# Kernel optimization log

Hardware: AMD Instinct MI355X
Metric: run time of the kernel (lower is better)

The kernel has to match this reference:

```python
import jax, jax.numpy as jnp
import numpy as np
from jax import lax

N_ENT = 20000; N_REL = 256; H = 512; C = 64; K = 3; L = 2; T = 8; E = 30000; B = 4096


def _seg_mean(vals, ids, num_segments):
    s = jax.ops.segment_sum(vals, ids, num_segments=num_segments)
    c = jax.ops.segment_sum(jnp.ones(ids.shape, vals.dtype), ids, num_segments=num_segments)
    return s / jnp.maximum(c, 1.0)[:, None]


def _normalize(x, eps=1e-8):
    return x / (jnp.linalg.norm(x, axis=-1, keepdims=True) + eps)


def _gru(x, h, Wih, Whh, bih, bhh):
    gi = x @ Wih + bih
    gh = h @ Whh + bhh
    ir, iz, inn = jnp.split(gi, 3, axis=-1)
    hr, hz, hn = jnp.split(gh, 3, axis=-1)
    r = jax.nn.sigmoid(ir + hr)
    z = jax.nn.sigmoid(iz + hz)
    n = jnp.tanh(inn + r * hn)
    return (1.0 - z) * n + z * h


def _backbone(x, convW, convB, fcW, fcB):
    # x: (B, Cin, H) -> (B, H); ConvTrans backbone: 1D 'same' conv over hidden dim,
    # relu, flatten, linear projection back to H, relu (BN identity at init, dropout=eval)
    h = lax.conv_general_dilated(x, convW, (1,), 'SAME', dimension_numbers=('NCH', 'OIH', 'NCH'))
    h = jax.nn.relu(h + convB[None, :, None])
    h = h.reshape(h.shape[0], -1)
    return jax.nn.relu(h @ fcW + fcB)


def _forward(ent_embeds, rel_embeds, W_msg, W_self, gru_Wih, gru_Whh, gru_bih, gru_bhh,
             gate_W, gate_b,
             e_conv1, e_cb1, e_fc1, e_fb1, e_conv2, e_cb2, e_fc2, e_fb2,
             r_conv1, r_cb1, r_fc1, r_fb1, r_conv2, r_cb2, r_fc2, r_fb2,
             src, dst, erel, subj, rel, obj):
    def step(carry, xs):
        ent, relh = carry
        s, d, r = xs
        # relation evolution: aggregate incident-entity embeds per relation, GRU with static rel embeds
        agg = _seg_mean(ent[s], r, N_REL)                                   # (R, H)
        relh = _gru(jnp.concatenate([agg, rel_embeds], -1), relh, gru_Wih, gru_Whh, gru_bih, gru_bhh)
        # entity evolution: L layers of RGCN-style message passing over the snapshot
        h = ent
        for l in range(L):
            msg = (h[s] + relh[r]) @ W_msg[l]                               # (E, H)
            h = jax.nn.relu(_seg_mean(msg, d, N_ENT) + h @ W_self[l])
        h = _normalize(h)
        u = jax.nn.sigmoid(h @ gate_W + gate_b)                             # time gate
        ent = u * h + (1.0 - u) * ent
        return (ent, relh), None

    (ent, relh), _ = lax.scan(step, (_normalize(ent_embeds), rel_embeds), (src, dst, erel))

    se = ent[subj]
    re_ = relh[rel]
    oe = ent[obj]
    # RefineConvTransE (object prediction)
    o1 = _backbone(jnp.stack([se, re_], 1), e_conv1, e_cb1, e_fc1, e_fb1)
    o2 = _backbone(jnp.stack([o1, se, re_], 1), e_conv2, e_cb2, e_fc2, e_fb2)
    # RefineConvTransR (relation prediction)
    q1 = _backbone(jnp.stack([se, oe], 1), r_conv1, r_cb1, r_fc1, r_fb1)
    q2 = _backbone(jnp.stack([q1, se, oe], 1), r_conv2, r_cb2, r_fc2, r_fb2)
    return (o1 @ ent.T, q1 @ relh.T, o2 @ ent.T, q2 @ relh.T)


def setup_inputs() -> dict:
    key = jax.random.key(0)
    ks = jax.random.split(key, 32)
    f = lambda i, shape, s=0.02: jax.random.normal(ks[i], shape, jnp.float32) * s
    return dict(
        ent_embeds=f(0, (N_ENT, H), 0.05),
        rel_embeds=f(1, (N_REL, H), 0.05),
        W_msg=f(2, (L, H, H)),
        W_self=f(3, (L, H, H)),
        gru_Wih=f(4, (2 * H, 3 * H)),
        gru_Whh=f(5, (H, 3 * H)),
        gru_bih=jnp.zeros((3 * H,), jnp.float32),
        gru_bhh=jnp.zeros((3 * H,), jnp.float32),
        gate_W=f(6, (H, H)),
        gate_b=jnp.zeros((H,), jnp.float32),
        e_conv1=f(7, (C, 2, K)), e_cb1=jnp.zeros((C,), jnp.float32),
        e_fc1=f(8, (C * H, H)), e_fb1=jnp.zeros((H,), jnp.float32),
        e_conv2=f(9, (C, 3, K)), e_cb2=jnp.zeros((C,), jnp.float32),
        e_fc2=f(10, (C * H, H)), e_fb2=jnp.zeros((H,), jnp.float32),
        r_conv1=f(11, (C, 2, K)), r_cb1=jnp.zeros((C,), jnp.float32),
        r_fc1=f(12, (C * H, H)), r_fb1=jnp.zeros((H,), jnp.float32),
        r_conv2=f(13, (C, 3, K)), r_cb2=jnp.zeros((C,), jnp.float32),
        r_fc2=f(14, (C * H, H)), r_fb2=jnp.zeros((H,), jnp.float32),
        src=jax.random.randint(ks[15], (T, E), 0, N_ENT),
        dst=jax.random.randint(ks[16], (T, E), 0, N_ENT),
        erel=jax.random.randint(ks[17], (T, E), 0, N_REL),
        subj=jax.random.randint(ks[18], (B,), 0, N_ENT),
        rel=jax.random.randint(ks[19], (B,), 0, N_REL),
        obj=jax.random.randint(ks[20], (B,), 0, N_ENT),
    )


def reference(ent_embeds, rel_embeds, W_msg, W_self, gru_Wih, gru_Whh, gru_bih, gru_bhh,
              gate_W, gate_b,
              e_conv1, e_cb1, e_fc1, e_fb1, e_conv2, e_cb2, e_fc2, e_fb2,
              r_conv1, r_cb1, r_fc1, r_fb1, r_conv2, r_cb2, r_fc2, r_fb2,
              src, dst, erel, subj, rel, obj):
    # returns (obj_logit_ori, rel_logit_ori, obj_logit, rel_logit)
    return _forward(ent_embeds, rel_embeds, W_msg, W_self, gru_Wih, gru_Whh, gru_bih, gru_bhh,
                    gate_W, gate_b,
                    e_conv1, e_cb1, e_fc1, e_fb1, e_conv2, e_cb2, e_fc2, e_fb2,
                    r_conv1, r_cb1, r_fc1, r_fb1, r_conv2, r_cb2, r_fc2, r_fb2,
                    src, dst, erel, subj, rel, obj)
```

## Files before the change

kernel.cpp:

```cpp
#include <hip/hip_runtime.h>
#include <math.h>


#define N_ENT 20000
#define N_REL 256
#define HD    512
#define NE    30000
#define NB    4096
#define NT    8

typedef __attribute__((ext_vector_type(8))) short          bf16x8;
typedef __attribute__((ext_vector_type(4))) float          f32x4;
typedef __attribute__((ext_vector_type(8))) unsigned short u16x8;
typedef __attribute__((ext_vector_type(4))) unsigned short u16x4;

static __device__ __forceinline__ float sigmoidf_(float x) {
  return 1.0f / (1.0f + expf(-x));
}
static __device__ __forceinline__ unsigned short f2bf(float f) {
  unsigned u = __float_as_uint(f);
  return (unsigned short)((u + 0x7FFFu + ((u >> 16) & 1u)) >> 16);
}

__global__ void rownorm_kernel(const float* __restrict__ in, float* __restrict__ out,
                               unsigned short* __restrict__ outb, int rows) {
  int wid = (blockIdx.x * blockDim.x + threadIdx.x) >> 6;
  int lane = threadIdx.x & 63;
  if (wid >= rows) return;
  const float4* ip = (const float4*)(in + (size_t)wid * HD);
  float4 v0 = ip[lane];
  float4 v1 = ip[lane + 64];
  float s = v0.x * v0.x + v0.y * v0.y + v0.z * v0.z + v0.w * v0.w
          + v1.x * v1.x + v1.y * v1.y + v1.z * v1.z + v1.w * v1.w;
  #pragma unroll
  for (int m = 1; m < 64; m <<= 1) s += __shfl_xor(s, m);
  float inv = 1.0f / (sqrtf(s) + 1e-8f);
  float4* op = (float4*)(out + (size_t)wid * HD);
  v0.x *= inv; v0.y *= inv; v0.z *= inv; v0.w *= inv;
  v1.x *= inv; v1.y *= inv; v1.z *= inv; v1.w *= inv;
  op[lane] = v0; op[lane + 64] = v1;
  unsigned short* ob = outb + (size_t)wid * HD;
  u16x4 p0 = {f2bf(v0.x), f2bf(v0.y), f2bf(v0.z), f2bf(v0.w)};
  u16x4 p1 = {f2bf(v1.x), f2bf(v1.y), f2bf(v1.z), f2bf(v1.w)};
  *(u16x4*)&ob[lane * 4] = p0;
  *(u16x4*)&ob[(lane + 64) * 4] = p1;
}

__global__ void zero_hist_all(int* __restrict__ h) {
  int i = blockIdx.x * 256 + threadIdx.x;
  if (i < NT * (N_ENT + N_REL)) h[i] = 0;
}

__global__ void hist_all(const int* __restrict__ dst, const int* __restrict__ rel,
                         int* __restrict__ histD8, int* __restrict__ histR8) {
  int e = blockIdx.x * 256 + threadIdx.x;
  int t = blockIdx.y;
  if (e >= NE) return;
  atomicAdd(&histD8[t * N_ENT + dst[t * NE + e]], 1);
  atomicAdd(&histR8[t * N_REL + rel[t * NE + e]], 1);
}

__global__ void scan_part_all(const int* __restrict__ histD8, int* __restrict__ partD8) {
  int t = blockIdx.x, tid = threadIdx.x;
  const int* hd = histD8 + t * N_ENT;
  int base = tid * 80;
  int s = 0;
  for (int i = 0; i < 80; ++i) {
    int idx = base + i;
    if (idx < N_ENT) s += hd[idx];
  }
  partD8[t * 257 + tid] = s;
}

__global__ void scan_serial_all(int* __restrict__ partD8, const int* __restrict__ histR8,
                                int* __restrict__ startR8, int* __restrict__ posR8) {
  int t = blockIdx.x;
  int* pd = partD8 + t * 257;
  int run = 0;
  for (int i = 0; i < 256; ++i) { int v = pd[i]; pd[i] = run; run += v; }
  pd[256] = run;
  const int* hr = histR8 + t * N_REL;
  int* sr = startR8 + t * 257;
  int* pr = posR8 + t * N_REL;
  run = 0;
  for (int i = 0; i < 256; ++i) { int v = hr[i]; sr[i] = run; pr[i] = run; run += v; }
  sr[256] = run;
}

__global__ void scan_local_all(const int* __restrict__ histD8, const int* __restrict__ partD8,
                               int* __restrict__ startD8, int* __restrict__ posD8) {
  int t = blockIdx.x, tid = threadIdx.x;
  const int* hd = histD8 + t * N_ENT;
  int* sd = startD8 + t * (N_ENT + 1);
  int* pd = posD8 + t * N_ENT;
  int run = partD8[t * 257 + tid];
  int base = tid * 80;
  for (int i = 0; i < 80; ++i) {
    int idx = base + i;
    if (idx < N_ENT) {
      sd[idx] = run;
      pd[idx] = run;
      run += hd[idx];
    }
  }
  if (tid == 0) sd[N_ENT] = partD8[t * 257 + 256];
}

__global__ void scatter_all(const int* __restrict__ dst, const int* __restrict__ rel,
                            int* __restrict__ posD8, int* __restrict__ posR8,
                            int* __restrict__ edgeD8, int* __restrict__ edgeR8) {
  int e = blockIdx.x * 256 + threadIdx.x;
  int t = blockIdx.y;
  if (e >= NE) return;
  int p = atomicAdd(&posD8[t * N_ENT + dst[t * NE + e]], 1);
  edgeD8[t * NE + p] = e;
  int p2 = atomicAdd(&posR8[t * N_REL + rel[t * NE + e]], 1);
  edgeR8[t * NE + p2] = e;
}

__global__ __launch_bounds__(256)
void agg_rel_csr(const float* __restrict__ ent, const int* __restrict__ src,
                 const int* __restrict__ edgeR, const int* __restrict__ startR,
                 float* __restrict__ aggR, float* __restrict__ cntR) {
  int r = blockIdx.x * 4 + (threadIdx.x >> 6);
  if (r >= N_REL) return;
  int lane = threadIdx.x & 63;
  int s0 = startR[r], s1 = startR[r + 1];
  float4 a = make_float4(0.f, 0.f, 0.f, 0.f);
  float4 b = make_float4(0.f, 0.f, 0.f, 0.f);
  for (int i = s0; i < s1; ++i) {
    int e = edgeR[i];
    int s = src[e];
    const float4* p = (const float4*)(ent + (size_t)s * HD);
    float4 x = p[lane];
    float4 y = p[lane + 64];
    a.x += x.x; a.y += x.y; a.z += x.z; a.w += x.w;
    b.x += y.x; b.y += y.y; b.z += y.z; b.w += y.w;
  }
  float4* op = (float4*)(aggR + (size_t)r * HD);
  op[lane] = a;
  op[lane + 64] = b;
  if (lane == 0) cntR[r] = (float)(s1 - s0);
}

__global__ __launch_bounds__(256)
void agg_ent_csr(const float* __restrict__ h, const float* __restrict__ relh,
                 const int* __restrict__ src, const int* __restrict__ erel,
                 const int* __restrict__ edgeD, const int* __restrict__ startD,
                 float* __restrict__ aggE, float* __restrict__ cntE) {
  int d = blockIdx.x * 4 + (threadIdx.x >> 6);
  if (d >= N_ENT) return;
  int lane = threadIdx.x & 63;
  int s0 = startD[d], s1 = startD[d + 1];
  float4 a = make_float4(0.f, 0.f, 0.f, 0.f);
  float4 b = make_float4(0.f, 0.f, 0.f, 0.f);
  for (int i = s0; i < s1; ++i) {
    int e = edgeD[i];
    int s = src[e], r = erel[e];
    const float4* hp = (const float4*)(h + (size_t)s * HD);
    const float4* rp = (const float4*)(relh + (size_t)r * HD);
    float4 x = hp[lane];
    float4 y = hp[lane + 64];
    float4 u = rp[lane];
    float4 v = rp[lane + 64];
    a.x += x.x + u.x; a.y += x.y + u.y; a.z += x.z + u.z; a.w += x.w + u.w;
    b.x += y.x + v.x; b.y += y.y + v.y; b.z += y.z + v.z; b.w += y.w + v.w;
  }
  float4* op = (float4*)(aggE + (size_t)d * HD);
  op[lane] = a;
  op[lane + 64] = b;
  if (lane == 0) cntE[d] = (float)(s1 - s0);
}

__global__ void gru_kernel(const float* __restrict__ gi, const float* __restrict__ gh,
                           const float* __restrict__ bih, const float* __restrict__ bhh,
                           float* __restrict__ relh, unsigned short* __restrict__ relhb) {
  int i = blockIdx.x * blockDim.x + threadIdx.x;
  if (i >= N_REL * HD) return;
  int row = i >> 9, col = i & 511;
  const float* gir = gi + (size_t)row * 1536;
  const float* ghr = gh + (size_t)row * 1536;
  float ir = gir[col] + bih[col];
  float iz = gir[col + 512] + bih[col + 512];
  float inn = gir[col + 1024] + bih[col + 1024];
  float hr = ghr[col] + bhh[col];
  float hz = ghr[col + 512] + bhh[col + 512];
  float hn = ghr[col + 1024] + bhh[col + 1024];
  float r = sigmoidf_(ir + hr);
  float z = sigmoidf_(iz + hz);
  float n = tanhf(inn + r * hn);
  float v = (1.0f - z) * n + z * relh[i];
  relh[i] = v;
  relhb[i] = f2bf(v);
}

__global__ void gather_kernel(const float* __restrict__ table, const int* __restrict__ idx,
                              float* __restrict__ out, int rows) {
  int i = blockIdx.x * blockDim.x + threadIdx.x;
  if (i >= rows * (HD / 4)) return;
  int row = i >> 7, q = i & 127;
  ((float4*)out)[i] = ((const float4*)(table + (size_t)idx[row] * HD))[q];
}

__global__ void f2b_kernel(const float* __restrict__ in, unsigned short* __restrict__ out, int n) {
  int i = blockIdx.x * blockDim.x + threadIdx.x;
  if (i * 8 >= n) return;
  float4 a = *(const float4*)&in[i * 8];
  float4 b = *(const float4*)&in[i * 8 + 4];
  u16x8 pk = {f2bf(a.x), f2bf(a.y), f2bf(a.z), f2bf(a.w),
              f2bf(b.x), f2bf(b.y), f2bf(b.z), f2bf(b.w)};
  *(u16x8*)&out[i * 8] = pk;
}

__global__ void pack_nn_kernel(const float* __restrict__ B, unsigned short* __restrict__ out,
                               int K, int N) {
  int id = blockIdx.x * 256 + threadIdx.x;
  if (id >= (K >> 3) * N) return;
  int s = id / (N * 4);
  int rem = id - s * (N * 4);
  int n = rem >> 2, g = rem & 3;
  const float* src = B + (size_t)(s * 32 + g * 8) * N + n;
  u16x8 pk;
  #pragma unroll
  for (int j = 0; j < 8; ++j) pk[j] = f2bf(src[(size_t)j * N]);
  *(u16x8*)&out[((size_t)s * N + n) * 32 + ((g ^ ((n >> 2) & 3)) << 3)] = pk;
}

template <int ACT, int MIRROR>
static __device__ __forceinline__
void gemm_core(const float* __restrict__ A0, int K0, const float* __restrict__ cntA,
               const unsigned short* __restrict__ A1, int K1,
               const unsigned short* __restrict__ Bp,
               const float* __restrict__ bias, const float* __restrict__ D,
               float* __restrict__ C, unsigned short* __restrict__ Cb,
               int M, int N, int m0, int n0,
               unsigned short (*As)[8192], unsigned short (*Bs)[8192]) {
  const int tid = threadIdx.x;
  const int lane = tid & 63;
  const int wv = tid >> 6;
  const int wm = wv >> 1, wn = wv & 1;
  const int lr = lane & 15, lg = lane >> 4;
  const int arow = tid >> 1;
  const int akh = (tid & 1) * 32;
  const int achunk = (tid & 1) * 4;
  const int NIT = (K0 + K1) >> 6;

  float s0 = 1.0f;
  if (K0 > 0 && (m0 + arow) < M) s0 = 1.0f / fmaxf(cntA[m0 + arow], 1.0f);

  f32x4 acc[4][4];
  #pragma unroll
  for (int i = 0; i < 4; ++i)
    #pragma unroll
    for (int j = 0; j < 4; ++j) acc[i][j] = (f32x4){0.f, 0.f, 0.f, 0.f};

  auto gload = [&](int it, u16x8* ar, u16x8* br) {
    int mrow = m0 + arow;
    int kk = it * 64 + akh;
    if (mrow < M) {
      if (kk < K0) {
        const float* p = A0 + (size_t)mrow * K0 + kk;
        #pragma unroll
        for (int q = 0; q < 4; ++q) {
          float4 x = *(const float4*)(p + q * 8);
          float4 y = *(const float4*)(p + q * 8 + 4);
          ar[q] = (u16x8){f2bf(x.x * s0), f2bf(x.y * s0), f2bf(x.z * s0), f2bf(x.w * s0),
                          f2bf(y.x * s0), f2bf(y.y * s0), f2bf(y.z * s0), f2bf(y.w * s0)};
        }
      } else {
        const unsigned short* p = A1 + (size_t)mrow * K1 + (kk - K0);
        #pragma unroll
        for (int q = 0; q < 4; ++q) ar[q] = *(const u16x8*)&p[q * 8];
      }
    } else {
      #pragma unroll
      for (int q = 0; q < 4; ++q) ar[q] = (u16x8){0, 0, 0, 0, 0, 0, 0, 0};
    }
    const unsigned short* b0 = Bp + ((size_t)(2 * it) * N + n0) * 32;
    const unsigned short* b1 = Bp + ((size_t)(2 * it + 1) * N + n0) * 32;
    br[0] = *(const u16x8*)&b0[tid * 8];
    br[1] = *(const u16x8*)&b0[2048 + tid * 8];
    br[2] = *(const u16x8*)&b1[tid * 8];
    br[3] = *(const u16x8*)&b1[2048 + tid * 8];
  };
  auto swrite = [&](int nb, const u16x8* ar, const u16x8* br) {
    #pragma unroll
    for (int q = 0; q < 4; ++q) {
      int chunk = achunk + q;
      *(u16x8*)&As[nb][arow * 64 + ((chunk ^ (arow & 7)) << 3)] = ar[q];
    }
    *(u16x8*)&Bs[nb][tid * 8] = br[0];
    *(u16x8*)&Bs[nb][2048 + tid * 8] = br[1];
    *(u16x8*)&Bs[nb][4096 + tid * 8] = br[2];
    *(u16x8*)&Bs[nb][4096 + 2048 + tid * 8] = br[3];
  };

  {
    u16x8 ar[4], br[4];
    gload(0, ar, br);
    swrite(0, ar, br);
  }
  __syncthreads();

  int cur = 0;
  for (int it = 0; it < NIT; ++it) {
    u16x8 ar[4], br[4];
    if (it + 1 < NIT) gload(it + 1, ar, br);
    bf16x8 af[2][4], bfr[2][4];
    #pragma unroll
    for (int u = 0; u < 2; ++u)
      #pragma unroll
      for (int i = 0; i < 4; ++i) {
        int r = wm * 64 + i * 16 + lr;
        af[u][i] = *(const bf16x8*)&As[cur][r * 64 + (((u * 4 + lg) ^ (r & 7)) << 3)];
        int nl = wn * 64 + i * 16 + lr;
        bfr[u][i] = *(const bf16x8*)&Bs[cur][u * 4096 + nl * 32 + ((lg ^ ((nl >> 2) & 3)) << 3)];
      }
    #pragma unroll
    for (int u = 0; u < 2; ++u)
      #pragma unroll
      for (int i = 0; i < 4; ++i)
        #pragma unroll
        for (int j = 0; j < 4; ++j)
          acc[i][j] = __builtin_amdgcn_mfma_f32_16x16x32_bf16(af[u][i], bfr[u][j], acc[i][j], 0, 0, 0);
    if (it + 1 < NIT) swrite(cur ^ 1, ar, br);
    __syncthreads();
    cur ^= 1;
  }

  #pragma unroll
  for (int i = 0; i < 4; ++i) {
    int m = m0 + wm * 64 + i * 16 + lg * 4;
    #pragma unroll
    for (int j = 0; j < 4; ++j) {
      int n = n0 + wn * 64 + j * 16 + lr;
      #pragma unroll
      for (int q = 0; q < 4; ++q) {
        int mr = m + q;
        if (mr >= M) continue;
        size_t o = (size_t)mr * N + n;
        float v = acc[i][j][q];
        if (ACT == 0) {
          C[o] = v;
        } else if (ACT == 1) {
          float rr = fmaxf(v, 0.0f);
          C[o] = rr;
          if (MIRROR) Cb[o] = f2bf(rr);
        } else {
          float u_ = sigmoidf_(v + bias[n]);
          float rr = u_ * D[o] + (1.0f - u_) * C[o];
          C[o] = rr;
          if (MIRROR) Cb[o] = f2bf(rr);
        }
      }
    }
  }
}

template <int ACT, int MIRROR>
__global__ __launch_bounds__(256, 2)
void gemm_nn2(const float* __restrict__ A0, int K0, const float* __restrict__ cntA,
              const unsigned short* __restrict__ A1, int K1,
              const unsigned short* __restrict__ Bp,
              const float* __restrict__ bias, const float* __restrict__ D,
              float* __restrict__ C, unsigned short* __restrict__ Cb, int M, int N) {
  __shared__ unsigned short As[2][8192];
  __shared__ unsigned short Bs[2][8192];
  gemm_core<ACT, MIRROR>(A0, K0, cntA, A1, K1, Bp, bias, D, C, Cb, M, N,
                         blockIdx.x * 128, blockIdx.y * 128, As, Bs);
}

__global__ __launch_bounds__(256, 2)
void gru_gemms(const float* __restrict__ aggR, const float* __restrict__ cntR,
               const unsigned short* __restrict__ rel_bf,
               const unsigned short* __restrict__ relh_bf,
               const unsigned short* __restrict__ wp_ih,
               const unsigned short* __restrict__ wp_hh,
               float* __restrict__ gi, float* __restrict__ gh) {
  __shared__ unsigned short As[2][8192];
  __shared__ unsigned short Bs[2][8192];
  if (blockIdx.z == 0)
    gemm_core<0, 0>(aggR, 512, cntR, rel_bf, 512, wp_ih, nullptr, nullptr,
                    gi, nullptr, N_REL, 1536, blockIdx.x * 128, blockIdx.y * 128, As, Bs);
  else
    gemm_core<0, 0>(nullptr, 0, nullptr, relh_bf, 512, wp_hh, nullptr, nullptr,
                    gh, nullptr, N_REL, 1536, blockIdx.x * 128, blockIdx.y * 128, As, Bs);
}

__global__ __launch_bounds__(256)
void pack_fw_kernel(const float* __restrict__ f0, const float* __restrict__ f1,
                    const float* __restrict__ f2, const float* __restrict__ f3,
                    unsigned short* __restrict__ o0, unsigned short* __restrict__ o1,
                    unsigned short* __restrict__ o2, unsigned short* __restrict__ o3) {
  __shared__ float L[32][512];
  const float* fw; unsigned short* op;
  switch (blockIdx.y) {
    case 0: fw = f0; op = o0; break;
    case 1: fw = f1; op = o1; break;
    case 2: fw = f2; op = o2; break;
    default: fw = f3; op = o3; break;
  }
  int s = blockIdx.x, tid = threadIdx.x;
  #pragma unroll
  for (int i = 0; i < 16; ++i) {
    int idx = tid + 256 * i;
    int r = idx >> 7, cq = (idx & 127) << 2;
    *(float4*)&L[r][cq] = *(const float4*)&fw[(size_t)(s * 32 + r) * 512 + cq];
  }
  __syncthreads();
  #pragma unroll
  for (int ii = 0; ii < 8; ++ii) {
    int slot = tid + 256 * ii;
    int n = slot >> 2, g = slot & 3;
    u16x8 pk;
    #pragma unroll
    for (int j = 0; j < 8; ++j) pk[j] = f2bf(L[g * 8 + j][n]);
    size_t off = (size_t)s * 16384 + n * 32 + ((g ^ ((n >> 2) & 3)) << 3);
    *(u16x8*)&op[off] = pk;
  }
}

template <int CIN>
__global__ __launch_bounds__(256)
void convgen_kernel(const float* __restrict__ X0e, const float* __restrict__ X1e,
                    const float* __restrict__ X2e,
                    const float* __restrict__ cwE, const float* __restrict__ cbE,
                    const float* __restrict__ X0r, const float* __restrict__ X1r,
                    const float* __restrict__ X2r,
                    const float* __restrict__ cwR, const float* __restrict__ cbR,
                    unsigned short* __restrict__ Ae, unsigned short* __restrict__ Ar) {
  __shared__ float wsm[64 * CIN * 3];
  __shared__ float bsm[64];
  const int path = blockIdx.y;
  const float* X[CIN]; const float* cw; const float* cb; unsigned short* A;
  if (path == 0) {
    X[0] = X0e; X[1] = X1e; if constexpr (CIN == 3) X[2] = X2e;
    cw = cwE; cb = cbE; A = Ae;
  } else {
    X[0] = X0r; X[1] = X1r; if constexpr (CIN == 3) X[2] = X2r;
    cw = cwR; cb = cbR; A = Ar;
  }
  const int tid = threadIdx.x;
  for (int i = tid; i < 64 * CIN * 3; i += 256) wsm[i] = cw[i];
  if (tid < 64) bsm[tid] = cb[tid];
  __syncthreads();

  const int o = tid & 63;
  const int b = blockIdx.x * 4 + (tid >> 6);
  const int h = o * 8;

  float xm[CIN][8], xl[CIN], xr[CIN];
  #pragma unroll
  for (int ci = 0; ci < CIN; ++ci) {
    const float* row = X[ci] + (size_t)b * HD + h;
    float4 a4 = *(const float4*)row;
    float4 b4 = *(const float4*)(row + 4);
    xm[ci][0] = a4.x; xm[ci][1] = a4.y; xm[ci][2] = a4.z; xm[ci][3] = a4.w;
    xm[ci][4] = b4.x; xm[ci][5] = b4.y; xm[ci][6] = b4.z; xm[ci][7] = b4.w;
    xl[ci] = (h > 0) ? row[-1] : 0.f;
    xr[ci] = (h + 8 < HD) ? row[8] : 0.f;
  }
  unsigned short* dst = A + (size_t)b * 32768 + h;
  for (int c = 0; c < 64; ++c) {
    float v[8];
    float cbv = bsm[c];
    #pragma unroll
    for (int e = 0; e < 8; ++e) v[e] = cbv;
    #pragma unroll
    for (int ci = 0; ci < CIN; ++ci) {
      float w0 = wsm[(c * CIN + ci) * 3 + 0];
      float w1 = wsm[(c * CIN + ci) * 3 + 1];
      float w2 = wsm[(c * CIN + ci) * 3 + 2];
      #pragma unroll
      for (int e = 0; e < 8; ++e) {
        float lft = e ? xm[ci][e - 1] : xl[ci];
        float rgt = (e < 7) ? xm[ci][e + 1] : xr[ci];
        v[e] = fmaf(lft, w0, fmaf(xm[ci][e], w1, fmaf(rgt, w2, v[e])));
      }
    }
    u16x8 pk;
    #pragma unroll
    for (int e = 0; e < 8; ++e) pk[e] = f2bf(fmaxf(v[e], 0.f));
    *(u16x8*)&dst[c * 512] = pk;
  }
}

__global__ __launch_bounds__(256, 2)
void gemm_fc(const unsigned short* __restrict__ Abuf,
             const unsigned short* __restrict__ fwpE,
             const unsigned short* __restrict__ fwpR,
             float* __restrict__ partBase) {
  __shared__ unsigned short As[2][128 * 64];
  __shared__ unsigned short Bs[2][2 * 128 * 32];
  const int tid = threadIdx.x;
  const int lane = tid & 63;
  const int wv = tid >> 6;
  const int wm = wv >> 1, wn = wv & 1;
  const int lr = lane & 15, lg = lane >> 4;
  const int m0 = blockIdx.x * 128;
  const int n0 = blockIdx.y * 128;
  const int path = blockIdx.z >> 2;
  const int ks = blockIdx.z & 3;

  const unsigned short* A = Abuf + (size_t)path * ((size_t)NB * 32768);
  const unsigned short* fwp = (path == 0) ? fwpE : fwpR;
  float* part = partBase + (size_t)(path * 4 + ks) * ((size_t)NB * HD);

  const int arow = tid >> 1;
  const int achunk = (tid & 1) * 4;
  const unsigned short* aRow = A + (size_t)(m0 + arow) * 32768 + ks * 8192 + achunk * 8;
  const unsigned short* bBase = fwp + (size_t)(ks * 256) * 16384 + (size_t)n0 * 32;

  f32x4 acc[4][4];
  #pragma unroll
  for (int i = 0; i < 4; ++i)
    #pragma unroll
    for (int j = 0; j < 4; ++j) acc[i][j] = (f32x4){0.f, 0.f, 0.f, 0.f};

  auto gload = [&](int it, u16x8* ar, u16x8* br) {
    const unsigned short* ap = aRow + it * 64;
    #pragma unroll
    for (int q = 0; q < 4; ++q) ar[q] = *(const u16x8*)&ap[q * 8];
    const unsigned short* bp = bBase + (size_t)it * 2 * 16384;
    br[0] = *(const u16x8*)&bp[tid * 8];
    br[1] = *(const u16x8*)&bp[2048 + tid * 8];
    br[2] = *(const u16x8*)&bp[16384 + tid * 8];
    br[3] = *(const u16x8*)&bp[16384 + 2048 + tid * 8];
  };
  auto swrite = [&](int nb, const u16x8* ar, const u16x8* br) {
    #pragma unroll
    for (int q = 0; q < 4; ++q) {
      int chunk = achunk + q;
      *(u16x8*)&As[nb][arow * 64 + ((chunk ^ (arow & 7)) << 3)] = ar[q];
    }
    *(u16x8*)&Bs[nb][tid * 8] = br[0];
    *(u16x8*)&Bs[nb][2048 + tid * 8] = br[1];
    *(u16x8*)&Bs[nb][4096 + tid * 8] = br[2];
    *(u16x8*)&Bs[nb][4096 + 2048 + tid * 8] = br[3];
  };
  auto mfma_phase = [&](int nb) {
    bf16x8 af[2][4], bfr[2][4];
    #pragma unroll
    for (int u = 0; u < 2; ++u)
      #pragma unroll
      for (int i = 0; i < 4; ++i) {
        int r = wm * 64 + i * 16 + lr;
        af[u][i] = *(const bf16x8*)&As[nb][r * 64 + (((u * 4 + lg) ^ (r & 7)) << 3)];
        int nl = wn * 64 + i * 16 + lr;
        bfr[u][i] = *(const bf16x8*)&Bs[nb][u * 4096 + nl * 32 + ((lg ^ ((nl >> 2) & 3)) << 3)];
      }
    #pragma unroll
    for (int u = 0; u < 2; ++u)
      #pragma unroll
      for (int i = 0; i < 4; ++i)
        #pragma unroll
        for (int j = 0; j < 4; ++j)
          acc[i][j] = __builtin_amdgcn_mfma_f32_16x16x32_bf16(af[u][i], bfr[u][j], acc[i][j], 0, 0, 0);
  };

  u16x8 ar0[4], br0[4], ar1[4], br1[4];
  gload(0, ar0, br0);
  swrite(0, ar0, br0);
  gload(1, ar1, br1);
  __syncthreads();

  int cur = 0;
  for (int itp = 0; itp < 128; itp += 2) {
    if (itp + 2 < 128) gload(itp + 2, ar0, br0);
    mfma_phase(cur);
    swrite(cur ^ 1, ar1, br1);
    __syncthreads();
    cur ^= 1;
    if (itp + 3 < 128) gload(itp + 3, ar1, br1);
    mfma_phase(cur);
    if (itp + 2 < 128) swrite(cur ^ 1, ar0, br0);
    __syncthreads();
    cur ^= 1;
  }

  #pragma unroll
  for (int i = 0; i < 4; ++i) {
    int m = m0 + wm * 64 + i * 16 + lg * 4;
    #pragma unroll
    for (int j = 0; j < 4; ++j) {
      int n = n0 + wn * 64 + j * 16 + lr;
      #pragma unroll
      for (int q = 0; q < 4; ++q)
        part[(size_t)(m + q) * HD + n] = acc[i][j][q];
    }
  }
}

__global__ void reduce4_kernel(const float* __restrict__ pE, const float* __restrict__ pR,
                               const float* __restrict__ bE, const float* __restrict__ bR,
                               float* __restrict__ oE, float* __restrict__ oR,
                               unsigned short* __restrict__ obE, unsigned short* __restrict__ obR) {
  int p = blockIdx.y;
  const float* part = p ? pR : pE;
  const float* bias = p ? bR : bE;
  float* o = p ? oR : oE;
  unsigned short* ob = p ? obR : obE;
  int i = blockIdx.x * 256 + threadIdx.x;
  int col = (i << 2) & 511;
  float4 s = *(const float4*)&part[(size_t)i * 4];
  #pragma unroll
  for (int ks = 1; ks < 4; ++ks) {
    float4 t = *(const float4*)&part[(size_t)ks * (NB * HD) + i * 4];
    s.x += t.x; s.y += t.y; s.z += t.z; s.w += t.w;
  }
  float4 b4 = *(const float4*)&bias[col];
  s.x = fmaxf(s.x + b4.x, 0.f); s.y = fmaxf(s.y + b4.y, 0.f);
  s.z = fmaxf(s.z + b4.z, 0.f); s.w = fmaxf(s.w + b4.w, 0.f);
  *(float4*)&o[(size_t)i * 4] = s;
  u16x4 pk = {f2bf(s.x), f2bf(s.y), f2bf(s.z), f2bf(s.w)};
  *(u16x4*)&ob[(size_t)i * 4] = pk;
}

__global__ __launch_bounds__(256, 3)
void gemm_nt_bf16(const unsigned short* __restrict__ A, const unsigned short* __restrict__ B,
                  float* __restrict__ C, int M, int N, int K) {
  __shared__ unsigned short As[128 * 64];
  __shared__ unsigned short Bs[128 * 64];
  const int tid = threadIdx.x;
  const int lane = tid & 63;
  const int w = tid >> 6;
  const int wm = w >> 1, wn = w & 1;
  const int m0 = blockIdx.x * 128, n0 = blockIdx.y * 128;
  const int lr = lane & 15, lg = lane >> 4;

  f32x4 acc[4][4];
  #pragma unroll
  for (int i = 0; i < 4; ++i)
    #pragma unroll
    for (int j = 0; j < 4; ++j) acc[i][j] = (f32x4){0.f, 0.f, 0.f, 0.f};

  for (int k0 = 0; k0 < K; k0 += 64) {
    __syncthreads();
    {
      int row = tid >> 1, half = tid & 1;
      const unsigned short* asrc = A + (size_t)(m0 + row) * K + k0 + half * 32;
      #pragma unroll
      for (int q = 0; q < 4; ++q) {
        int chunk = half * 4 + q;
        *(u16x8*)&As[row * 64 + (chunk ^ (row & 7)) * 8] = *(const u16x8*)&asrc[q * 8];
      }
      int nrow = n0 + row;
      const unsigned short* bsrc = B + (size_t)nrow * K + k0 + half * 32;
      u16x8 z = {0, 0, 0, 0, 0, 0, 0, 0};
      #pragma unroll
      for (int q = 0; q < 4; ++q) {
        int chunk = half * 4 + q;
        u16x8 v = (nrow < N) ? *(const u16x8*)&bsrc[q * 8] : z;
        *(u16x8*)&Bs[row * 64 + (chunk ^ (row & 7)) * 8] = v;
      }
    }
    __syncthreads();
    #pragma unroll
    for (int u = 0; u < 2; ++u) {
      bf16x8 a[4], b[4];
      #pragma unroll
      for (int i = 0; i < 4; ++i) {
        int r = wm * 64 + i * 16 + lr;
        a[i] = *(const bf16x8*)&As[r * 64 + (((u * 4 + lg) ^ (r & 7))) * 8];
        int n = wn * 64 + i * 16 + lr;
        b[i] = *(const bf16x8*)&Bs[n * 64 + (((u * 4 + lg) ^ (n & 7))) * 8];
      }
      #pragma unroll
      for (int i = 0; i < 4; ++i)
        #pragma unroll
        for (int j = 0; j < 4; ++j)
          acc[i][j] = __builtin_amdgcn_mfma_f32_16x16x32_bf16(a[i], b[j], acc[i][j], 0, 0, 0);
    }
  }

  #pragma unroll
  for (int i = 0; i < 4; ++i) {
    int m = m0 + wm * 64 + i * 16 + lg * 4;
    #pragma unroll
    for (int j = 0; j < 4; ++j) {
      int n = n0 + wn * 64 + j * 16 + lr;
      if (n < N) {
        #pragma unroll
        for (int q = 0; q < 4; ++q)
          C[(size_t)(m + q) * N + n] = acc[i][j][q];
      }
    }
  }
}

extern "C" void kernel_launch(void* const* d_in, const int* in_sizes, int n_in,
                              void* d_out, int out_size, void* d_ws, size_t ws_size,
                              hipStream_t stream) {
  const float* ent_embeds = (const float*)d_in[0];
  const float* rel_embeds = (const float*)d_in[1];
  const float* W_msg  = (const float*)d_in[2];
  const float* W_self = (const float*)d_in[3];
  const float* gru_Wih = (const float*)d_in[4];
  const float* gru_Whh = (const float*)d_in[5];
  const float* gru_bih = (const float*)d_in[6];
  const float* gru_bhh = (const float*)d_in[7];
  const float* gate_W = (const float*)d_in[8];
  const float* gate_b = (const float*)d_in[9];
  const float* e_conv1 = (const float*)d_in[10]; const float* e_cb1 = (const float*)d_in[11];
  const float* e_fc1   = (const float*)d_in[12]; const float* e_fb1 = (const float*)d_in[13];
  const float* e_conv2 = (const float*)d_in[14]; const float* e_cb2 = (const float*)d_in[15];
  const float* e_fc2   = (const float*)d_in[16]; const float* e_fb2 = (const float*)d_in[17];
  const float* r_conv1 = (const float*)d_in[18]; const float* r_cb1 = (const float*)d_in[19];
  const float* r_fc1   = (const float*)d_in[20]; const float* r_fb1 = (const float*)d_in[21];
  const float* r_conv2 = (const float*)d_in[22]; const float* r_cb2 = (const float*)d_in[23];
  const float* r_fc2   = (const float*)d_in[24]; const float* r_fb2 = (const float*)d_in[25];
  const int* src  = (const int*)d_in[26];
  const int* dst  = (const int*)d_in[27];
  const int* erel = (const int*)d_in[28];
  const int* subj = (const int*)d_in[29];
  const int* rel  = (const int*)d_in[30];
  const int* obj  = (const int*)d_in[31];
  float* out = (float*)d_out;

  float* w = (float*)d_ws;
  float* ent   = w; w += (size_t)N_ENT * HD;
  float* relh  = w; w += (size_t)N_REL * HD;
  float* aggR  = w; w += (size_t)N_REL * HD;
  float* cntR  = w; w += N_REL;
  float* gi    = w; w += (size_t)N_REL * 1536;
  float* gh    = w; w += (size_t)N_REL * 1536;
  float* aggE  = w; w += (size_t)N_ENT * HD;
  float* cntE  = w; w += N_ENT;
  float* tmp   = w; w += (size_t)N_ENT * HD;
  float* h0b   = w; w += (size_t)N_ENT * HD;
  float* h1b   = w; w += (size_t)N_ENT * HD;
  float* se    = w; w += (size_t)NB * HD;
  float* re_   = w; w += (size_t)NB * HD;
  float* oe    = w; w += (size_t)NB * HD;
  float* o1    = w; w += (size_t)NB * HD;
  float* q1    = w; w += (size_t)NB * HD;
  float* o2    = w; w += (size_t)NB * HD;
  float* q2    = w; w += (size_t)NB * HD;
  unsigned short* ent_bf  = (unsigned short*)w; w += (size_t)N_ENT * HD / 2;
  unsigned short* relh_bf = (unsigned short*)w; w += (size_t)N_REL * HD / 2;
  unsigned short* rel_bf  = (unsigned short*)w; w += (size_t)N_REL * HD / 2;
  unsigned short* h0b_bf  = (unsigned short*)w; w += (size_t)N_ENT * HD / 2;
  unsigned short* h1b_bf  = (unsigned short*)w; w += (size_t)N_ENT * HD / 2;
  unsigned short* o1b = (unsigned short*)w; w += (size_t)NB * HD / 2;
  unsigned short* q1b = (unsigned short*)w; w += (size_t)NB * HD / 2;
  unsigned short* o2b = (unsigned short*)w; w += (size_t)NB * HD / 2;
  unsigned short* q2b = (unsigned short*)w; w += (size_t)NB * HD / 2;
  unsigned short* wp_ih = (unsigned short*)w;
  unsigned short* wp_hh = wp_ih + (size_t)1024 * 1536;
  unsigned short* wp_l0 = wp_hh + (size_t)512 * 1536;
  unsigned short* wp_l1 = wp_l0 + (size_t)1024 * 512;
  unsigned short* wp_g  = wp_l1 + (size_t)1024 * 512;
  w += ((size_t)1024 * 1536 + 512 * 1536 + 2 * 1024 * 512 + 512 * 512) / 2;
  int* histD8  = (int*)w;
  int* histR8  = histD8 + (size_t)NT * N_ENT;
  int* partD8  = histR8 + (size_t)NT * N_REL;
  int* startD8 = partD8 + (size_t)NT * 257;
  int* posD8   = startD8 + (size_t)NT * (N_ENT + 1);
  int* startR8 = posD8 + (size_t)NT * N_ENT;
  int* posR8   = startR8 + (size_t)NT * 257;
  int* edgeD8  = posR8 + (size_t)NT * N_REL;
  int* edgeR8  = edgeD8 + (size_t)NT * NE;
  unsigned short* fwp0 = (unsigned short*)aggE;
  unsigned short* fwp1 = fwp0 + (size_t)16777216;
  unsigned short* fwp2 = fwp1 + (size_t)16777216;
  unsigned short* fwp3 = fwp2 + (size_t)16777216;
  (void)tmp;
  unsigned short* Abuf = (unsigned short*)out;
  float* pE = out + (size_t)2 * NB * 32768 / 2;
  float* pR = pE + (size_t)4 * NB * HD;

  const dim3 g_gru(2, 12, 2);
  const dim3 g_ent(157, 4);

  {
    int t;
    t = (1024 * 1536) / 8; pack_nn_kernel<<<(t + 255) / 256, 256, 0, stream>>>(gru_Wih, wp_ih, 1024, 1536);
    t = (512 * 1536) / 8;  pack_nn_kernel<<<(t + 255) / 256, 256, 0, stream>>>(gru_Whh, wp_hh, 512, 1536);
    t = (512 * 512) / 8;
    pack_nn_kernel<<<(t + 255) / 256, 256, 0, stream>>>(W_msg, wp_l0, 512, 512);
    pack_nn_kernel<<<(t + 255) / 256, 256, 0, stream>>>(W_self, wp_l0 + (size_t)512 * 512, 512, 512);
    pack_nn_kernel<<<(t + 255) / 256, 256, 0, stream>>>(W_msg + (size_t)512 * 512, wp_l1, 512, 512);
    pack_nn_kernel<<<(t + 255) / 256, 256, 0, stream>>>(W_self + (size_t)512 * 512, wp_l1 + (size_t)512 * 512, 512, 512);
    pack_nn_kernel<<<(t + 255) / 256, 256, 0, stream>>>(gate_W, wp_g, 512, 512);
  }

  zero_hist_all<<<(NT * (N_ENT + N_REL) + 255) / 256, 256, 0, stream>>>(histD8);
  hist_all<<<dim3((NE + 255) / 256, NT), 256, 0, stream>>>(dst, erel, histD8, histR8);
  scan_part_all<<<NT, 256, 0, stream>>>(histD8, partD8);
  scan_serial_all<<<NT, 1, 0, stream>>>(partD8, histR8, startR8, posR8);
  scan_local_all<<<NT, 256, 0, stream>>>(histD8, partD8, startD8, posD8);
  scatter_all<<<dim3((NE + 255) / 256, NT), 256, 0, stream>>>(dst, erel, posD8, posR8,
                                                              edgeD8, edgeR8);

  rownorm_kernel<<<N_ENT / 4, 256, 0, stream>>>(ent_embeds, ent, ent_bf, N_ENT);
  hipMemcpyAsync(relh, rel_embeds, (size_t)N_REL * HD * 4, hipMemcpyDeviceToDevice, stream);
  f2b_kernel<<<(N_REL * HD / 8) / 256, 256, 0, stream>>>(rel_embeds, rel_bf, N_REL * HD);
  f2b_kernel<<<(N_REL * HD / 8) / 256, 256, 0, stream>>>(rel_embeds, relh_bf, N_REL * HD);

  for (int t = 0; t < NT; ++t) {
    const int* st = src + t * NE;
    const int* rt = erel + t * NE;
    const int* edgeD = edgeD8 + (size_t)t * NE;
    const int* edgeR = edgeR8 + (size_t)t * NE;
    const int* startD = startD8 + (size_t)t * (N_ENT + 1);
    const int* startR = startR8 + (size_t)t * 257;

    agg_rel_csr<<<N_REL / 4, 256, 0, stream>>>(ent, st, edgeR, startR, aggR, cntR);
    gru_gemms<<<g_gru, 256, 0, stream>>>(aggR, cntR, rel_bf, relh_bf, wp_ih, wp_hh, gi, gh);
    gru_kernel<<<(N_REL * HD) / 256, 256, 0, stream>>>(gi, gh, gru_bih, gru_bhh, relh, relh_bf);

    agg_ent_csr<<<N_ENT / 4, 256, 0, stream>>>(ent, relh, st, rt, edgeD, startD, aggE, cntE);
    gemm_nn2<1, 1><<<g_ent, 256, 0, stream>>>(aggE, 512, cntE, ent_bf, 512, wp_l0,
                                              nullptr, nullptr, h0b, h0b_bf, N_ENT, 512);
    agg_ent_csr<<<N_ENT / 4, 256, 0, stream>>>(h0b, relh, st, rt, edgeD, startD, aggE, cntE);
    gemm_nn2<1, 0><<<g_ent, 256, 0, stream>>>(aggE, 512, cntE, h0b_bf, 512, wp_l1,
                                              nullptr, nullptr, h1b, nullptr, N_ENT, 512);
    rownorm_kernel<<<N_ENT / 4, 256, 0, stream>>>(h1b, h1b, h1b_bf, N_ENT);
    gemm_nn2<3, 1><<<g_ent, 256, 0, stream>>>(nullptr, 0, nullptr, h1b_bf, 512, wp_g,
                                              gate_b, h1b, ent, ent_bf, N_ENT, 512);
  }

  pack_fw_kernel<<<dim3(1024, 4), 256, 0, stream>>>(e_fc1, r_fc1, e_fc2, r_fc2,
                                                    fwp0, fwp1, fwp2, fwp3);
  gather_kernel<<<(NB * HD / 4) / 256, 256, 0, stream>>>(ent, subj, se, NB);
  gather_kernel<<<(NB * HD / 4) / 256, 256, 0, stream>>>(relh, rel, re_, NB);
  gather_kernel<<<(NB * HD / 4) / 256, 256, 0, stream>>>(ent, obj, oe, NB);

  unsigned short* A_E = Abuf;
  unsigned short* A_R = Abuf + (size_t)NB * 32768;

  convgen_kernel<2><<<dim3(NB / 4, 2), 256, 0, stream>>>(
      se, re_, nullptr, e_conv1, e_cb1,
      se, oe, nullptr, r_conv1, r_cb1, A_E, A_R);
  gemm_fc<<<dim3(32, 4, 8), 256, 0, stream>>>(Abuf, fwp0, fwp1, pE);
  reduce4_kernel<<<dim3(NB * HD / 4 / 256, 2), 256, 0, stream>>>(
      pE, pR, e_fb1, r_fb1, o1, q1, o1b, q1b);

  convgen_kernel<3><<<dim3(NB / 4, 2), 256, 0, stream>>>(
      o1, se, re_, e_conv2, e_cb2,
      q1, se, oe, r_conv2, r_cb2, A_E, A_R);
  gemm_fc<<<dim3(32, 4, 8), 256, 0, stream>>>(Abuf, fwp2, fwp3, pE);
  reduce4_kernel<<<dim3(NB * HD / 4 / 256, 2), 256, 0, stream>>>(
      pE, pR, e_fb2, r_fb2, o2, q2, o2b, q2b);

  size_t off0 = 0;
  size_t off1 = (size_t)NB * N_ENT;
  size_t off2 = off1 + (size_t)NB * N_REL;
  size_t off3 = off2 + (size_t)NB * N_ENT;
  gemm_nt_bf16<<<dim3(32, 157), 256, 0, stream>>>(o1b, ent_bf, out + off0, NB, N_ENT, HD);
  gemm_nt_bf16<<<dim3(32, 2), 256, 0, stream>>>(q1b, relh_bf, out + off1, NB, N_REL, HD);
  gemm_nt_bf16<<<dim3(32, 157), 256, 0, stream>>>(o2b, ent_bf, out + off2, NB, N_ENT, HD);
  gemm_nt_bf16<<<dim3(32, 2), 256, 0, stream>>>(q2b, relh_bf, out + off3, NB, N_REL, HD);
}
```

Baseline: 4.642 ms.

## Deepen GEMM prefetch to two register stages and double-buffer the NT GEMM

The first bf16 GEMM loop is restructured to keep two K-tiles of global loads in flight in registers, unrolling the loop by two so each tile's loads overlap two MFMA phases. The NT GEMM, which previously loaded shared memory synchronously with two barriers per tile, gets the same double-buffered LDS plus two-deep register prefetch scheme. The goal is to hide global-memory latency behind matrix math, at the cost of more registers and LDS, so the NT kernel's occupancy bound drops from 3 to 2 blocks. The pipeline assumes an even tile count along K.

```diff
diff --git a/kernel.cpp b/kernel.cpp
--- a/kernel.cpp
+++ b/kernel.cpp
@@ -294,27 +294,16 @@
     *(u16x8*)&Bs[nb][4096 + tid * 8] = br[2];
     *(u16x8*)&Bs[nb][4096 + 2048 + tid * 8] = br[3];
   };
-
-  {
-    u16x8 ar[4], br[4];
-    gload(0, ar, br);
-    swrite(0, ar, br);
-  }
-  __syncthreads();
-
-  int cur = 0;
-  for (int it = 0; it < NIT; ++it) {
-    u16x8 ar[4], br[4];
-    if (it + 1 < NIT) gload(it + 1, ar, br);
+  auto mfma_phase = [&](int nb) {
     bf16x8 af[2][4], bfr[2][4];
     #pragma unroll
     for (int u = 0; u < 2; ++u)
       #pragma unroll
       for (int i = 0; i < 4; ++i) {
         int r = wm * 64 + i * 16 + lr;
-        af[u][i] = *(const bf16x8*)&As[cur][r * 64 + (((u * 4 + lg) ^ (r & 7)) << 3)];
+        af[u][i] = *(const bf16x8*)&As[nb][r * 64 + (((u * 4 + lg) ^ (r & 7)) << 3)];
         int nl = wn * 64 + i * 16 + lr;
-        bfr[u][i] = *(const bf16x8*)&Bs[cur][u * 4096 + nl * 32 + ((lg ^ ((nl >> 2) & 3)) << 3)];
+        bfr[u][i] = *(const bf16x8*)&Bs[nb][u * 4096 + nl * 32 + ((lg ^ ((nl >> 2) & 3)) << 3)];
       }
     #pragma unroll
     for (int u = 0; u < 2; ++u)
@@ -323,7 +312,24 @@
         #pragma unroll
         for (int j = 0; j < 4; ++j)
           acc[i][j] = __builtin_amdgcn_mfma_f32_16x16x32_bf16(af[u][i], bfr[u][j], acc[i][j], 0, 0, 0);
-    if (it + 1 < NIT) swrite(cur ^ 1, ar, br);
+  };
+
+  u16x8 ar0[4], br0[4], ar1[4], br1[4];
+  gload(0, ar0, br0);
+  swrite(0, ar0, br0);
+  gload(1, ar1, br1);
+  __syncthreads();
+
+  int cur = 0;
+  for (int itp = 0; itp < NIT; itp += 2) {
+    if (itp + 2 < NIT) gload(itp + 2, ar0, br0);
+    mfma_phase(cur);
+    swrite(cur ^ 1, ar1, br1);
+    __syncthreads();
+    cur ^= 1;
+    if (itp + 3 < NIT) gload(itp + 3, ar1, br1);
+    mfma_phase(cur);
+    if (itp + 2 < NIT) swrite(cur ^ 1, ar0, br0);
     __syncthreads();
     cur ^= 1;
   }
@@ -616,17 +622,20 @@
   *(u16x4*)&ob[(size_t)i * 4] = pk;
 }
 
-__global__ __launch_bounds__(256, 3)
+__global__ __launch_bounds__(256, 2)
 void gemm_nt_bf16(const unsigned short* __restrict__ A, const unsigned short* __restrict__ B,
                   float* __restrict__ C, int M, int N, int K) {
-  __shared__ unsigned short As[128 * 64];
-  __shared__ unsigned short Bs[128 * 64];
+  __shared__ unsigned short As[2][8192];
+  __shared__ unsigned short Bs[2][8192];
   const int tid = threadIdx.x;
   const int lane = tid & 63;
-  const int w = tid >> 6;
-  const int wm = w >> 1, wn = w & 1;
+  const int wv = tid >> 6;
+  const int wm = wv >> 1, wn = wv & 1;
   const int m0 = blockIdx.x * 128, n0 = blockIdx.y * 128;
   const int lr = lane & 15, lg = lane >> 4;
+  const int row = tid >> 1, half = tid & 1;
+  const int nrow = n0 + row;
+  const int NIT = K >> 6;
 
   f32x4 acc[4][4];
   #pragma unroll
@@ -634,36 +643,33 @@
     #pragma unroll
     for (int j = 0; j < 4; ++j) acc[i][j] = (f32x4){0.f, 0.f, 0.f, 0.f};
 
-  for (int k0 = 0; k0 < K; k0 += 64) {
-    __syncthreads();
-    {
-      int row = tid >> 1, half = tid & 1;
-      const unsigned short* asrc = A + (size_t)(m0 + row) * K + k0 + half * 32;
-      #pragma unroll
-      for (int q = 0; q < 4; ++q) {
-        int chunk = half * 4 + q;
-        *(u16x8*)&As[row * 64 + (chunk ^ (row & 7)) * 8] = *(const u16x8*)&asrc[q * 8];
-      }
-      int nrow = n0 + row;
-      const unsigned short* bsrc = B + (size_t)nrow * K + k0 + half * 32;
-      u16x8 z = {0, 0, 0, 0, 0, 0, 0, 0};
-      #pragma unroll
-      for (int q = 0; q < 4; ++q) {
-        int chunk = half * 4 + q;
-        u16x8 v = (nrow < N) ? *(const u16x8*)&bsrc[q * 8] : z;
-        *(u16x8*)&Bs[row * 64 + (chunk ^ (row & 7)) * 8] = v;
-      }
-    }
-    __syncthreads();
+  auto gload = [&](int it, u16x8* ar, u16x8* br) {
+    const unsigned short* asrc = A + (size_t)(m0 + row) * K + it * 64 + half * 32;
+    #pragma unroll
+    for (int q = 0; q < 4; ++q) ar[q] = *(const u16x8*)&asrc[q * 8];
+    const unsigned short* bsrc = B + (size_t)nrow * K + it * 64 + half * 32;
+    u16x8 z = {0, 0, 0, 0, 0, 0, 0, 0};
+    #pragma unroll
+    for (int q = 0; q < 4; ++q) br[q] = (nrow < N) ? *(const u16x8*)&bsrc[q * 8] : z;
+  };
+  auto swrite = [&](int nb, const u16x8* ar, const u16x8* br) {
+    #pragma unroll
+    for (int q = 0; q < 4; ++q) {
+      int chunk = half * 4 + q;
+      *(u16x8*)&As[nb][row * 64 + ((chunk ^ (row & 7)) << 3)] = ar[q];
+      *(u16x8*)&Bs[nb][row * 64 + ((chunk ^ (row & 7)) << 3)] = br[q];
+    }
+  };
+  auto mfma_phase = [&](int nb) {
     #pragma unroll
     for (int u = 0; u < 2; ++u) {
       bf16x8 a[4], b[4];
       #pragma unroll
       for (int i = 0; i < 4; ++i) {
         int r = wm * 64 + i * 16 + lr;
-        a[i] = *(const bf16x8*)&As[r * 64 + (((u * 4 + lg) ^ (r & 7))) * 8];
+        a[i] = *(const bf16x8*)&As[nb][r * 64 + (((u * 4 + lg) ^ (r & 7)) << 3)];
         int n = wn * 64 + i * 16 + lr;
-        b[i] = *(const bf16x8*)&Bs[n * 64 + (((u * 4 + lg) ^ (n & 7))) * 8];
+        b[i] = *(const bf16x8*)&Bs[nb][n * 64 + (((u * 4 + lg) ^ (n & 7)) << 3)];
       }
       #pragma unroll
       for (int i = 0; i < 4; ++i)
@@ -671,6 +677,26 @@
         for (int j = 0; j < 4; ++j)
           acc[i][j] = __builtin_amdgcn_mfma_f32_16x16x32_bf16(a[i], b[j], acc[i][j], 0, 0, 0);
     }
+  };
+
+  u16x8 ar0[4], br0[4], ar1[4], br1[4];
+  gload(0, ar0, br0);
+  swrite(0, ar0, br0);
+  gload(1, ar1, br1);
+  __syncthreads();
+
+  int cur = 0;
+  for (int itp = 0; itp < NIT; itp += 2) {
+    if (itp + 2 < NIT) gload(itp + 2, ar0, br0);
+    mfma_phase(cur);
+    swrite(cur ^ 1, ar1, br1);
+    __syncthreads();
+    cur ^= 1;
+    if (itp + 3 < NIT) gload(itp + 3, ar1, br1);
+    mfma_phase(cur);
+    if (itp + 2 < NIT) swrite(cur ^ 1, ar0, br0);
+    __syncthreads();
+    cur ^= 1;
   }
 
   #pragma unroll
```

Result: faster. 4.531 ms (-2.4%).
